# Performance work log

Hardware: AMD Instinct MI355X
Metric: run time of the kernel (lower is better)

## Reference

```python
import jax, jax.numpy as jnp
import numpy as np

N_NODES = 100000
N_EDGES = 1600000
D = 64  # in = hidden = out channels


def setup_inputs() -> dict:
    key = jax.random.key(0)
    ks = jax.random.split(key, 12)
    x = jax.random.normal(ks[0], (N_NODES, D), dtype=jnp.float32)
    src = jax.random.randint(ks[1], (N_EDGES,), 0, N_NODES, dtype=jnp.int32)
    dst = jax.random.randint(ks[2], (N_EDGES,), 0, N_NODES, dtype=jnp.int32)
    s = 1.0 / np.sqrt(D)
    params = {}
    for i in range(3):
        params[f"Wl{i}"] = jax.random.uniform(ks[3 + 3 * i], (D, D), jnp.float32, -s, s)
        params[f"bl{i}"] = jax.random.uniform(ks[4 + 3 * i], (D,), jnp.float32, -s, s)
        params[f"Wr{i}"] = jax.random.uniform(ks[5 + 3 * i], (D, D), jnp.float32, -s, s)
    return {"x": x, "src": src, "dst": dst, **params}


def _sage_conv(x, src, dst, Wl, bl, Wr):
    # mean aggregation of source-node features into destination nodes
    agg = jax.ops.segment_sum(x[src], dst, num_segments=N_NODES)          # [N, D]
    deg = jax.ops.segment_sum(jnp.ones((src.shape[0], 1), x.dtype), dst,
                              num_segments=N_NODES)                        # [N, 1]
    mean = agg / jnp.maximum(deg, 1.0)
    # PyG SAGEConv: lin_l(mean_neigh) + lin_r(x_root); lin_l has bias, lin_r does not
    return mean @ Wl.T + bl + x @ Wr.T


def reference(x, src, dst, Wl0, bl0, Wr0, Wl1, bl1, Wr1, Wl2, bl2, Wr2):
    h = jax.nn.relu(_sage_conv(x, src, dst, Wl0, bl0, Wr0))  # dropout no-op (eval)
    h = jax.nn.relu(_sage_conv(h, src, dst, Wl1, bl1, Wr1))
    return _sage_conv(h, src, dst, Wl2, bl2, Wr2)
```

## Files before the change

### kernel.cpp

```cpp
#include <hip/hip_runtime.h>

#define NN 100000
#define NE 1600000
#define D 64

#define NBUCK ((NN + 255) / 256)
#define EPB 4096
#define P1_BLOCKS ((NE + EPB - 1) / EPB)
#define BCAP 6144

#define F2BF_BLOCKS (NN * 16 / 256)
#define WPREP_BLOCKS (3 * 64 * 128 / 256)

typedef __attribute__((ext_vector_type(8))) short bfrag;
typedef __attribute__((ext_vector_type(4))) float f4acc;

__device__ __forceinline__ unsigned short f2bf(float f) {
    unsigned u = __float_as_uint(f);
    u = (u + 0x7FFFu + ((u >> 16) & 1u)) >> 16;
    return (unsigned short)u;
}

__global__ __launch_bounds__(256) void p1prep_kernel(
    const int* __restrict__ src, const int* __restrict__ dst,
    int* __restrict__ bucket_cur, unsigned* __restrict__ packed,
    const float* __restrict__ x, unsigned short* __restrict__ xb,
    const float* __restrict__ Wl0, const float* __restrict__ Wr0,
    const float* __restrict__ Wl1, const float* __restrict__ Wr1,
    const float* __restrict__ Wl2, const float* __restrict__ Wr2,
    unsigned short* __restrict__ wcat) {
    int b = blockIdx.x;
    int t = threadIdx.x;
    if (b >= P1_BLOCKS) {
        int pb = b - P1_BLOCKS;
        if (pb < F2BF_BLOCKS) {
            int i = pb * 256 + t;
            float4 v = ((const float4*)x)[i];
            ushort4 o;
            o.x = f2bf(v.x); o.y = f2bf(v.y); o.z = f2bf(v.z); o.w = f2bf(v.w);
            ((ushort4*)xb)[i] = o;
        } else {
            int i = (pb - F2BF_BLOCKS) * 256 + t;
            int layer = i >> 13;
            int rem = i & 8191;
            int n = rem >> 7;
            int k = rem & 127;
            const float* W;
            if (layer == 0) W = (k < 64) ? Wl0 : Wr0;
            else if (layer == 1) W = (k < 64) ? Wl1 : Wr1;
            else W = (k < 64) ? Wl2 : Wr2;
            wcat[i] = f2bf(W[n * 64 + (k & 63)]);
        }
        return;
    }
    __shared__ int h[NBUCK];
    __shared__ int ls[512];
    __shared__ int lstart[NBUCK];
    __shared__ int lcur[NBUCK];
    __shared__ unsigned sl[EPB];
    __shared__ unsigned short sb[EPB];
    for (int i = t; i < NBUCK; i += 256) h[i] = 0;
    __syncthreads();
    int base = b * EPB;
    int cnt = min(EPB, NE - base);
    for (int i = t; i < cnt; i += 256) atomicAdd(&h[dst[base + i] >> 8], 1);
    __syncthreads();
    ls[t] = h[t];
    ls[t + 256] = (t + 256 < NBUCK) ? h[t + 256] : 0;
    __syncthreads();
    for (int off = 1; off < 512; off <<= 1) {
        int a = (t >= off) ? ls[t - off] : 0;
        int b2 = (t + 256 >= off) ? ls[t + 256 - off] : 0;
        __syncthreads();
        ls[t] += a;
        ls[t + 256] += b2;
        __syncthreads();
    }
    for (int i = t; i < NBUCK; i += 256) {
        int c = h[i];
        int excl = ls[i] - c;
        lstart[i] = excl;
        lcur[i] = excl;
        h[i] = c ? atomicAdd(&bucket_cur[i], c) : 0;
    }
    __syncthreads();
    for (int i = t; i < cnt; i += 256) {
        int d = dst[base + i];
        int bk = d >> 8;
        int pos = atomicAdd(&lcur[bk], 1);
        sl[pos] = ((unsigned)(d & 255) << 24) | (unsigned)src[base + i];
        sb[pos] = (unsigned short)bk;
    }
    __syncthreads();
    for (int j = t; j < cnt; j += 256) {
        int bk = sb[j];
        packed[bk * BCAP + h[bk] + (j - lstart[bk])] = sl[j];
    }
}

__global__ __launch_bounds__(256) void p2b_place(const unsigned* __restrict__ packed,
                                                 const int* __restrict__ bucket_cur,
                                                 int2* __restrict__ rowpair,
                                                 int* __restrict__ esrc, int nNodes) {
    __shared__ int h[256];
    __shared__ int cur[256];
    __shared__ int sl[BCAP];
    int b = blockIdx.x, t = threadIdx.x;
    h[t] = 0;
    __syncthreads();
    int lo = b * BCAP;
    int cnt = bucket_cur[b];
    for (int i = t; i < cnt; i += 256) atomicAdd(&h[packed[lo + i] >> 24], 1);
    __syncthreads();
    int v = h[t];
    for (int off = 1; off < 256; off <<= 1) {
        int u = (t >= off) ? h[t - off] : 0;
        __syncthreads();
        h[t] += u;
        __syncthreads();
    }
    int incl = h[t];
    int excl = incl - v;
    cur[t] = excl;
    int node = b * 256 + t;
    if (node < nNodes) rowpair[node] = make_int2(lo + excl, lo + incl);
    __syncthreads();
    for (int i = t; i < cnt; i += 256) {
        unsigned p = packed[lo + i];
        int pos = atomicAdd(&cur[p >> 24], 1);
        if (pos < BCAP) sl[pos] = (int)(p & 0xFFFFFFu);
    }
    __syncthreads();
    for (int i = t; i < cnt; i += 256) esrc[lo + i] = sl[i];
    if (t < 16 && cnt + t < BCAP) esrc[lo + cnt + t] = 0;
}

__global__ __launch_bounds__(256) void sage_layer(
    const unsigned short* __restrict__ xb,
    const int2* __restrict__ rowpair, const int* __restrict__ esrc,
    const unsigned short* __restrict__ wcat,
    const float* __restrict__ bl,
    float* __restrict__ outF,
    unsigned short* __restrict__ outB,
    int nNodes, int doRelu) {
    __shared__ unsigned short smean[32 * 64];
    __shared__ float tf[32 * 64];

    int t = threadIdx.x;
    {
        int nl = t >> 3;
        int q = t & 7;
        int lane = t & 63;
        int gbase = lane & 56;
        int node = blockIdx.x * 32 + nl;
        uint4 o = make_uint4(0, 0, 0, 0);
        if (node < nNodes) {
            int2 rp = rowpair[node];
            int rs = rp.x;
            int re = rp.y;
            float a0 = 0, a1 = 0, a2 = 0, a3 = 0, a4 = 0, a5 = 0, a6 = 0, a7 = 0;
            for (int i = rs; i < re; i += 16) {
                int mA = esrc[i + q];
                int mB = esrc[i + 8 + q];
                int rem = re - i;
                int s[16];
#pragma unroll
                for (int j = 0; j < 16; ++j) {
                    int jj = min(j, rem - 1);
                    int sa = __shfl(mA, gbase + (jj & 7), 64);
                    int sb2 = __shfl(mB, gbase + (jj & 7), 64);
                    s[j] = (jj < 8) ? sa : sb2;
                }
#pragma unroll
                for (int j = 0; j < 16; ++j) {
                    uint4 w = ((const uint4*)xb)[s[j] * 8 + q];
                    if (i + j < re) {
                        a0 += __uint_as_float(w.x << 16);
                        a1 += __uint_as_float(w.x & 0xFFFF0000u);
                        a2 += __uint_as_float(w.y << 16);
                        a3 += __uint_as_float(w.y & 0xFFFF0000u);
                        a4 += __uint_as_float(w.z << 16);
                        a5 += __uint_as_float(w.z & 0xFFFF0000u);
                        a6 += __uint_as_float(w.w << 16);
                        a7 += __uint_as_float(w.w & 0xFFFF0000u);
                    }
                }
            }
            float inv = 1.0f / fmaxf((float)(re - rs), 1.0f);
            o.x = (unsigned)f2bf(a0 * inv) | ((unsigned)f2bf(a1 * inv) << 16);
            o.y = (unsigned)f2bf(a2 * inv) | ((unsigned)f2bf(a3 * inv) << 16);
            o.z = (unsigned)f2bf(a4 * inv) | ((unsigned)f2bf(a5 * inv) << 16);
            o.w = (unsigned)f2bf(a6 * inv) | ((unsigned)f2bf(a7 * inv) << 16);
        }
        int idx = nl * 64 + ((q * 8) ^ ((nl & 7) << 3));
        *(uint4*)&smean[idx] = o;
    }
    __syncthreads();

    int w = t >> 6;
    int l = t & 63;
    int lr = l & 15;
    int lk = l >> 4;

    const bfrag* wB = (const bfrag*)wcat;
    int n = w * 16 + lr;
    bfrag b0 = wB[n * 16 + lk];
    bfrag b1 = wB[n * 16 + 4 + lk];
    bfrag b2 = wB[n * 16 + 8 + lk];
    bfrag b3 = wB[n * 16 + 12 + lk];
    float bias = bl[n];

    int base = blockIdx.x * 32;
    f4acc accv[2];
#pragma unroll
    for (int rt = 0; rt < 2; ++rt) {
        int row0 = base + rt * 16;
        int lrow = rt * 16 + lr;
        int sw = (lrow & 7) << 3;
        bfrag a0 = *(const bfrag*)&smean[lrow * 64 + ((lk * 8) ^ sw)];
        bfrag a1 = *(const bfrag*)&smean[lrow * 64 + ((32 + lk * 8) ^ sw)];
        int grow = row0 + lr;
        if (grow >= nNodes) grow = nNodes - 1;
        const bfrag* xr = (const bfrag*)(xb + (size_t)grow * D);
        bfrag a2 = xr[lk];
        bfrag a3 = xr[4 + lk];
        f4acc acc = {0.f, 0.f, 0.f, 0.f};
        acc = __builtin_amdgcn_mfma_f32_16x16x32_bf16(a0, b0, acc, 0, 0, 0);
        acc = __builtin_amdgcn_mfma_f32_16x16x32_bf16(a1, b1, acc, 0, 0, 0);
        acc = __builtin_amdgcn_mfma_f32_16x16x32_bf16(a2, b2, acc, 0, 0, 0);
        acc = __builtin_amdgcn_mfma_f32_16x16x32_bf16(a3, b3, acc, 0, 0, 0);
        accv[rt] = acc;
    }
    __syncthreads();

    if (outB) {
#pragma unroll
        for (int rt = 0; rt < 2; ++rt)
#pragma unroll
            for (int r = 0; r < 4; ++r) {
                int row = rt * 16 + lk * 4 + r;
                float v = accv[rt][r] + bias;
                if (doRelu) v = fmaxf(v, 0.f);
                smean[row * 64 + (n ^ ((row & 7) << 3))] = f2bf(v);
            }
        __syncthreads();
        int row = t >> 3;
        int node = base + row;
        int c8 = t & 7;
        if (node < nNodes) {
            uint4 v = *(uint4*)&smean[row * 64 + ((c8 ^ (row & 7)) * 8)];
            ((uint4*)outB)[(size_t)node * 8 + c8] = v;
        }
    } else {
#pragma unroll
        for (int rt = 0; rt < 2; ++rt)
#pragma unroll
            for (int r = 0; r < 4; ++r) {
                int row = rt * 16 + lk * 4 + r;
                float v = accv[rt][r] + bias;
                if (doRelu) v = fmaxf(v, 0.f);
                tf[row * 64 + (n ^ ((row & 7) << 3))] = v;
            }
        __syncthreads();
        int row = t >> 3;
        int node = base + row;
        int c8 = t & 7;
        if (node < nNodes) {
            int cs = (c8 ^ (row & 7)) * 8;
            float4 v0 = *(float4*)&tf[row * 64 + cs];
            float4 v1 = *(float4*)&tf[row * 64 + cs + 4];
            ((float4*)outF)[(size_t)node * 16 + c8 * 2 + 0] = v0;
            ((float4*)outF)[(size_t)node * 16 + c8 * 2 + 1] = v1;
        }
    }
}

extern "C" void kernel_launch(void* const* d_in, const int* in_sizes, int n_in,
                              void* d_out, int out_size, void* d_ws, size_t ws_size,
                              hipStream_t stream) {
    const float* x   = (const float*)d_in[0];
    const int*   src = (const int*)d_in[1];
    const int*   dst = (const int*)d_in[2];
    const float* Wl0 = (const float*)d_in[3];
    const float* bl0 = (const float*)d_in[4];
    const float* Wr0 = (const float*)d_in[5];
    const float* Wl1 = (const float*)d_in[6];
    const float* bl1 = (const float*)d_in[7];
    const float* Wr1 = (const float*)d_in[8];
    const float* Wl2 = (const float*)d_in[9];
    const float* bl2 = (const float*)d_in[10];
    const float* Wr2 = (const float*)d_in[11];
    float* out = (float*)d_out;

    const size_t MB = 1 << 20;
    char* ws = (char*)d_ws;
    int* bucket_cur = (int*)(ws);
    unsigned short* wcat = (unsigned short*)(ws + (128 << 10));
    int2* rowpair = (int2*)(ws + 1 * MB);
    int* esrc   = (int*)(ws + 2 * MB);
    unsigned* packed = (unsigned*)(ws + 12 * MB);
    unsigned short* hbA = (unsigned short*)(ws + 12 * MB);
    unsigned short* xb  = (unsigned short*)(ws + 26 * MB);
    unsigned short* hbB = (unsigned short*)(ws + 39 * MB);

    hipMemsetAsync(bucket_cur, 0, (size_t)NBUCK * sizeof(int), stream);

    p1prep_kernel<<<P1_BLOCKS + F2BF_BLOCKS + WPREP_BLOCKS, 256, 0, stream>>>(
        src, dst, bucket_cur, packed, x, xb, Wl0, Wr0, Wl1, Wr1, Wl2, Wr2, wcat);
    p2b_place<<<NBUCK, 256, 0, stream>>>(packed, bucket_cur, rowpair, esrc, NN);

    const int layerGrid = (NN + 31) / 32;
    sage_layer<<<layerGrid, 256, 0, stream>>>(xb,  rowpair, esrc, wcat,         bl0, nullptr, hbA, NN, 1);
    sage_layer<<<layerGrid, 256, 0, stream>>>(hbA, rowpair, esrc, wcat + 8192,  bl1, nullptr, hbB, NN, 1);
    sage_layer<<<layerGrid, 256, 0, stream>>>(hbB, rowpair, esrc, wcat + 16384, bl2, out, nullptr, NN, 0);
}
```

Before: 177.5 us.

## Sort nodes by degree within each bucket to balance gather work per wave

Inside the bucket placement kernel, nodes are binned by in-degree through a small shared-memory histogram and prefix scan, and a node permutation is written in which each 256-node bucket is ordered by degree. The layer kernels take their 32 nodes from this permutation, so the 8-thread groups in a wave gather similar edge counts and wait less on the longest neighbour list. The cost is an extra indirection for each node index, scattered row reads and writes instead of contiguous ones, and some extra scan work during placement.

```diff
diff --git a/kernel.cpp b/kernel.cpp
--- a/kernel.cpp
+++ b/kernel.cpp
@@ -101,12 +101,17 @@
 __global__ __launch_bounds__(256) void p2b_place(const unsigned* __restrict__ packed,
                                                  const int* __restrict__ bucket_cur,
                                                  int2* __restrict__ rowpair,
-                                                 int* __restrict__ esrc, int nNodes) {
+                                                 int* __restrict__ esrc,
+                                                 int* __restrict__ nodeperm, int nNodes) {
     __shared__ int h[256];
     __shared__ int cur[256];
     __shared__ int sl[BCAP];
+    __shared__ int dh[64];
+    __shared__ int dls[64];
+    __shared__ int dcur[64];
     int b = blockIdx.x, t = threadIdx.x;
     h[t] = 0;
+    if (t < 64) dh[t] = 0;
     __syncthreads();
     int lo = b * BCAP;
     int cnt = bucket_cur[b];
@@ -123,14 +128,34 @@
     int excl = incl - v;
     cur[t] = excl;
     int node = b * 256 + t;
-    if (node < nNodes) rowpair[node] = make_int2(lo + excl, lo + incl);
+    bool valid = node < nNodes;
+    int bin = min(v, 63);
+    if (valid) {
+        rowpair[node] = make_int2(lo + excl, lo + incl);
+        atomicAdd(&dh[bin], 1);
+    }
     __syncthreads();
     for (int i = t; i < cnt; i += 256) {
         unsigned p = packed[lo + i];
         int pos = atomicAdd(&cur[p >> 24], 1);
         if (pos < BCAP) sl[pos] = (int)(p & 0xFFFFFFu);
     }
-    __syncthreads();
+    if (t < 64) dls[t] = dh[t];
+    __syncthreads();
+    for (int off = 1; off < 64; off <<= 1) {
+        int u = (t >= off && t < 64) ? dls[t - off] : 0;
+        __syncthreads();
+        if (t < 64) dls[t] += u;
+        __syncthreads();
+    }
+    if (t < 64) dcur[t] = dls[t] - dh[t];
+    __syncthreads();
+    if (valid) {
+        int pos = atomicAdd(&dcur[bin], 1);
+        nodeperm[b * 256 + pos] = node;
+    } else {
+        nodeperm[b * 256 + t] = -1;
+    }
     for (int i = t; i < cnt; i += 256) esrc[lo + i] = sl[i];
     if (t < 16 && cnt + t < BCAP) esrc[lo + cnt + t] = 0;
 }
@@ -138,6 +163,7 @@
 __global__ __launch_bounds__(256) void sage_layer(
     const unsigned short* __restrict__ xb,
     const int2* __restrict__ rowpair, const int* __restrict__ esrc,
+    const int* __restrict__ nodeperm,
     const unsigned short* __restrict__ wcat,
     const float* __restrict__ bl,
     float* __restrict__ outF,
@@ -147,14 +173,15 @@
     __shared__ float tf[32 * 64];
 
     int t = threadIdx.x;
+    int pbase = blockIdx.x * 32;
     {
         int nl = t >> 3;
         int q = t & 7;
         int lane = t & 63;
         int gbase = lane & 56;
-        int node = blockIdx.x * 32 + nl;
+        int node = nodeperm[pbase + nl];
         uint4 o = make_uint4(0, 0, 0, 0);
-        if (node < nNodes) {
+        if (node >= 0) {
             int2 rp = rowpair[node];
             int rs = rp.x;
             int re = rp.y;
@@ -210,18 +237,16 @@
     bfrag b3 = wB[n * 16 + 12 + lk];
     float bias = bl[n];
 
-    int base = blockIdx.x * 32;
     f4acc accv[2];
 #pragma unroll
     for (int rt = 0; rt < 2; ++rt) {
-        int row0 = base + rt * 16;
         int lrow = rt * 16 + lr;
         int sw = (lrow & 7) << 3;
         bfrag a0 = *(const bfrag*)&smean[lrow * 64 + ((lk * 8) ^ sw)];
         bfrag a1 = *(const bfrag*)&smean[lrow * 64 + ((32 + lk * 8) ^ sw)];
-        int grow = row0 + lr;
-        if (grow >= nNodes) grow = nNodes - 1;
-        const bfrag* xr = (const bfrag*)(xb + (size_t)grow * D);
+        int gnode = nodeperm[pbase + lrow];
+        if (gnode < 0) gnode = 0;
+        const bfrag* xr = (const bfrag*)(xb + (size_t)gnode * D);
         bfrag a2 = xr[lk];
         bfrag a3 = xr[4 + lk];
         f4acc acc = {0.f, 0.f, 0.f, 0.f};
@@ -245,9 +270,9 @@
             }
         __syncthreads();
         int row = t >> 3;
-        int node = base + row;
+        int node = nodeperm[pbase + row];
         int c8 = t & 7;
-        if (node < nNodes) {
+        if (node >= 0) {
             uint4 v = *(uint4*)&smean[row * 64 + ((c8 ^ (row & 7)) * 8)];
             ((uint4*)outB)[(size_t)node * 8 + c8] = v;
         }
@@ -263,9 +288,9 @@
             }
         __syncthreads();
         int row = t >> 3;
-        int node = base + row;
+        int node = nodeperm[pbase + row];
         int c8 = t & 7;
-        if (node < nNodes) {
+        if (node >= 0) {
             int cs = (c8 ^ (row & 7)) * 8;
             float4 v0 = *(float4*)&tf[row * 64 + cs];
             float4 v1 = *(float4*)&tf[row * 64 + cs + 4];
@@ -298,19 +323,20 @@
     unsigned short* wcat = (unsigned short*)(ws + (128 << 10));
     int2* rowpair = (int2*)(ws + 1 * MB);
     int* esrc   = (int*)(ws + 2 * MB);
-    unsigned* packed = (unsigned*)(ws + 12 * MB);
-    unsigned short* hbA = (unsigned short*)(ws + 12 * MB);
-    unsigned short* xb  = (unsigned short*)(ws + 26 * MB);
-    unsigned short* hbB = (unsigned short*)(ws + 39 * MB);
+    int* nodeperm = (int*)(ws + 2 * MB + (size_t)NBUCK * BCAP * 4);
+    unsigned* packed = (unsigned*)(ws + 13 * MB);
+    unsigned short* hbA = (unsigned short*)(ws + 13 * MB);
+    unsigned short* xb  = (unsigned short*)(ws + 27 * MB);
+    unsigned short* hbB = (unsigned short*)(ws + 40 * MB);
 
     hipMemsetAsync(bucket_cur, 0, (size_t)NBUCK * sizeof(int), stream);
 
     p1prep_kernel<<<P1_BLOCKS + F2BF_BLOCKS + WPREP_BLOCKS, 256, 0, stream>>>(
         src, dst, bucket_cur, packed, x, xb, Wl0, Wr0, Wl1, Wr1, Wl2, Wr2, wcat);
-    p2b_place<<<NBUCK, 256, 0, stream>>>(packed, bucket_cur, rowpair, esrc, NN);
-
-    const int layerGrid = (NN + 31) / 32;
-    sage_layer<<<layerGrid, 256, 0, stream>>>(xb,  rowpair, esrc, wcat,         bl0, nullptr, hbA, NN, 1);
-    sage_layer<<<layerGrid, 256, 0, stream>>>(hbA, rowpair, esrc, wcat + 8192,  bl1, nullptr, hbB, NN, 1);
-    sage_layer<<<layerGrid, 256, 0, stream>>>(hbB, rowpair, esrc, wcat + 16384, bl2, out, nullptr, NN, 0);
-}
+    p2b_place<<<NBUCK, 256, 0, stream>>>(packed, bucket_cur, rowpair, esrc, nodeperm, NN);
+
+    const int layerGrid = NBUCK * 8;
+    sage_layer<<<layerGrid, 256, 0, stream>>>(xb,  rowpair, esrc, nodeperm, wcat,         bl0, nullptr, hbA, NN, 1);
+    sage_layer<<<layerGrid, 256, 0, stream>>>(hbA, rowpair, esrc, nodeperm, wcat + 8192,  bl1, nullptr, hbB, NN, 1);
+    sage_layer<<<layerGrid, 256, 0, stream>>>(hbB, rowpair, esrc, nodeperm, wcat + 16384, bl2, out, nullptr, NN, 0);
+}
```

New measurement: 196.2 us. +10.6%, slower.
